# Performance work log

Measured on AMD Instinct MI355X. Metric: run time of the kernel, lower is better.

## Reference

```python
import jax, jax.numpy as jnp
import numpy as np

B, T, C = 32, 128, 64
E, H = 8, 4            # feat_dim, num_heads
D = E // H             # head_dim = 2
HID = 32               # hidden_dim


def setup_inputs() -> dict:
    key = jax.random.key(0)
    ks = jax.random.split(key, 20)
    s = 0.1
    return {
        "x": jax.random.normal(ks[0], (B, T, C), jnp.float32),
        # input_proj: Linear(C, C)
        "W_in": jax.random.normal(ks[1], (C, C), jnp.float32) * s,
        "b_in": jax.random.normal(ks[2], (C,), jnp.float32) * s,
        # time_step_score: Linear(C, C//4) -> GELU -> Linear(C//4, 1) -> Sigmoid
        "W_ts1": jax.random.normal(ks[3], (C // 4, C), jnp.float32) * s,
        "b_ts1": jax.random.normal(ks[4], (C // 4,), jnp.float32) * s,
        "W_ts2": jax.random.normal(ks[5], (1, C // 4), jnp.float32) * s,
        "b_ts2": jax.random.normal(ks[6], (1,), jnp.float32) * s,
        # per-channel GRU(1 -> E): torch gate order (r, z, n)
        "W_ih": jax.random.normal(ks[7], (C, 3 * E), jnp.float32) * s,      # input size 1
        "W_hh": jax.random.normal(ks[8], (C, 3 * E, E), jnp.float32) * s,
        "b_ih": jax.random.normal(ks[9], (C, 3 * E), jnp.float32) * s,
        "b_hh": jax.random.normal(ks[10], (C, 3 * E), jnp.float32) * s,
        # shared MultiheadAttention(E, 4): packed in_proj + out_proj
        "W_qkv": jax.random.normal(ks[11], (3 * E, E), jnp.float32) * s,
        "b_qkv": jax.random.normal(ks[12], (3 * E,), jnp.float32) * s,
        "W_o": jax.random.normal(ks[13], (E, E), jnp.float32) * s,
        "b_o": jax.random.normal(ks[14], (E,), jnp.float32) * s,
        # out_proj: Linear(C*E, HID)
        "W_out": jax.random.normal(ks[15], (HID, C * E), jnp.float32) * s,
        "b_out": jax.random.normal(ks[16], (HID,), jnp.float32) * s,
    }


def _forward(x, W_in, b_in, W_ts1, b_ts1, W_ts2, b_ts2,
             W_ih, W_hh, b_ih, b_hh, W_qkv, b_qkv, W_o, b_o, W_out, b_out):
    bs, ts, c = x.shape
    # time step importance: per-timestep MLP over the raw features
    h1 = jax.nn.gelu(jnp.einsum('btc,fc->btf', x, W_ts1) + b_ts1, approximate=False)
    ts_imp = jax.nn.sigmoid(jnp.einsum('btf,of->bto', h1, W_ts2) + b_ts2)[..., 0]  # [B,T]

    xp = jnp.einsum('btc,dc->btd', x, W_in) + b_in  # [B,T,C]

    # Batched per-channel GRU scan over time. state h: [B,C,E]
    def step(h, x_t):
        gi = x_t[:, :, None] * W_ih[None] + b_ih          # [B,C,3E]
        gh = jnp.einsum('bce,cge->bcg', h, W_hh) + b_hh   # [B,C,3E]
        ir, iz, inn = gi[..., :E], gi[..., E:2 * E], gi[..., 2 * E:]
        hr, hz, hn = gh[..., :E], gh[..., E:2 * E], gh[..., 2 * E:]
        r = jax.nn.sigmoid(ir + hr)
        z = jax.nn.sigmoid(iz + hz)
        n = jnp.tanh(inn + r * hn)
        h_new = (1.0 - z) * n + z * h
        return h_new, h_new

    h0 = jnp.zeros((bs, c, E), xp.dtype)
    _, hs = jax.lax.scan(step, h0, jnp.transpose(xp, (1, 0, 2)))  # [T,B,C,E]
    hs_bcte = jnp.transpose(hs, (1, 2, 0, 3))                     # [B,C,T,E]

    # Shared MHA applied independently per channel (batched over B*C)
    qkv = jnp.einsum('bcte,fe->bctf', hs_bcte, W_qkv) + b_qkv     # [B,C,T,3E]
    q, k, v = qkv[..., :E], qkv[..., E:2 * E], qkv[..., 2 * E:]
    def heads(t):
        return t.reshape(bs, c, ts, H, D)
    q, k, v = heads(q), heads(k), heads(v)
    scores = jnp.einsum('bcthd,bcshd->bchts', q, k) / np.sqrt(D)
    attn = jax.nn.softmax(scores, axis=-1)
    o = jnp.einsum('bchts,bcshd->bcthd', attn, v).reshape(bs, c, ts, E)
    attn_out = jnp.einsum('bcte,fe->bctf', o, W_o) + b_o          # [B,C,T,E]
    attention = jnp.transpose(attn_out, (0, 2, 1, 3))             # [B,T,C,E]

    out_flat = jnp.transpose(hs, (1, 0, 2, 3)).reshape(bs, ts, c * E)  # [B,T,C*E]
    out = jnp.einsum('btf,hf->bth', out_flat, W_out) + b_out           # [B,T,HID]

    feat_imp = jax.nn.sigmoid(attention.sum(axis=(1, 3)))   # [B,C]
    tsf_imp = jax.nn.sigmoid(attention.sum(axis=-1))        # [B,T,C]
    return out[:, -1, :], feat_imp, ts_imp, tsf_imp


def reference(x, W_in, b_in, W_ts1, b_ts1, W_ts2, b_ts2,
              W_ih, W_hh, b_ih, b_hh, W_qkv, b_qkv, W_o, b_o, W_out, b_out):
    return _forward(x, W_in, b_in, W_ts1, b_ts1, W_ts2, b_ts2,
                    W_ih, W_hh, b_ih, b_hh, W_qkv, b_qkv, W_o, b_o, W_out, b_out)
```

## Files before the change

### kernel.cpp

```cpp
#include <hip/hip_runtime.h>
#include <hip/hip_bf16.h>
#include <math.h>

#define B_ 32
#define T_ 128
#define C_ 64
#define E_ 8
#define HID_ 32

__device__ __forceinline__ float sigmoidf_(float x) { return 1.0f / (1.0f + __expf(-x)); }
__device__ __forceinline__ float tanhf_(float x) {
    float xc = fminf(fmaxf(x, -15.0f), 15.0f);
    float e = __expf(2.0f * xc);
    return (e - 1.0f) / (e + 1.0f);
}

__global__ __launch_bounds__(128) void k_attn_f(
    const float* __restrict__ x, const float* __restrict__ W_in, const float* __restrict__ b_in,
    const float* __restrict__ W_ih, const float* __restrict__ W_hh,
    const float* __restrict__ b_ih, const float* __restrict__ b_hh,
    const float* __restrict__ W_qkv, const float* __restrict__ b_qkv,
    const float* __restrict__ W_o, const float* __restrict__ b_o,
    float* __restrict__ fh,
    float* __restrict__ feat_imp, float* __restrict__ tsf_imp)
{
    const int bc = blockIdx.x;
    const int b = bc >> 6, c = bc & 63;
    const int tid = threadIdx.x;

    __shared__ __align__(16) float ks[T_][E_];
    __shared__ __align__(16) float vs[T_][E_];
    __shared__ __align__(16) float hsl[T_][E_];
    __shared__ __align__(16) float xcol[T_];
    __shared__ __align__(16) float win_c[C_];

    if (tid < C_) win_c[tid] = W_in[c * C_ + tid];
    __syncthreads();

    {
        float a = b_in[c];
        const float4* xr = (const float4*)(x + (b * T_ + tid) * C_);
        const float4* wv4 = (const float4*)win_c;
#pragma unroll
        for (int k4 = 0; k4 < 16; ++k4) {
            float4 xv = xr[k4];
            float4 wv = wv4[k4];
            a = fmaf(xv.x, wv.x, a); a = fmaf(xv.y, wv.y, a);
            a = fmaf(xv.z, wv.z, a); a = fmaf(xv.w, wv.w, a);
        }
        xcol[tid] = a;
    }
    __syncthreads();

    if (tid < E_) {
        const int e = tid;
        float wr[E_], wz[E_], wn[E_];
#pragma unroll
        for (int j = 0; j < E_; ++j) {
            wr[j] = W_hh[(c * 24 + 0 * E_ + e) * E_ + j];
            wz[j] = W_hh[(c * 24 + 1 * E_ + e) * E_ + j];
            wn[j] = W_hh[(c * 24 + 2 * E_ + e) * E_ + j];
        }
        const float wir = W_ih[c * 24 + e], wiz = W_ih[c * 24 + E_ + e], win = W_ih[c * 24 + 2 * E_ + e];
        const float bir = b_ih[c * 24 + e], biz = b_ih[c * 24 + E_ + e], bin_ = b_ih[c * 24 + 2 * E_ + e];
        const float bhr = b_hh[c * 24 + e], bhz = b_hh[c * 24 + E_ + e], bhn = b_hh[c * 24 + 2 * E_ + e];

        float h = 0.0f;
        for (int t = 0; t < T_; ++t) {
            float xv = xcol[t];
            float gr = fmaf(xv, wir, bir) + bhr;
            float gz = fmaf(xv, wiz, biz) + bhz;
            float gn = fmaf(xv, win, bin_);
            float hn = bhn;
#pragma unroll
            for (int j = 0; j < E_; ++j) {
                float hj = __shfl(h, j, E_);
                gr = fmaf(hj, wr[j], gr);
                gz = fmaf(hj, wz[j], gz);
                hn = fmaf(hj, wn[j], hn);
            }
            float r = sigmoidf_(gr);
            float z = sigmoidf_(gz);
            float nn = tanhf_(fmaf(r, hn, gn));
            h = (1.0f - z) * nn + z * h;
            hsl[t][e] = h;
        }
        fh[bc * E_ + e] = h;
    }
    __syncthreads();

    const int t = tid;
    float hrow[E_];
#pragma unroll
    for (int j = 0; j < E_; ++j) hrow[j] = hsl[t][j];

    float q[E_];
#pragma unroll
    for (int f = 0; f < E_; ++f) {
        float a = b_qkv[f];
#pragma unroll
        for (int j = 0; j < E_; ++j) a = fmaf(hrow[j], W_qkv[f * E_ + j], a);
        q[f] = a;
    }
#pragma unroll
    for (int f = 0; f < E_; ++f) {
        float a = b_qkv[E_ + f];
#pragma unroll
        for (int j = 0; j < E_; ++j) a = fmaf(hrow[j], W_qkv[(E_ + f) * E_ + j], a);
        ks[t][f] = a;
    }
#pragma unroll
    for (int f = 0; f < E_; ++f) {
        float a = b_qkv[2 * E_ + f];
#pragma unroll
        for (int j = 0; j < E_; ++j) a = fmaf(hrow[j], W_qkv[(2 * E_ + f) * E_ + j], a);
        vs[t][f] = a;
    }
    __syncthreads();

    const float scale = 0.70710678118654752f;
    float l[4] = {0.f, 0.f, 0.f, 0.f};
    float acc[E_] = {0.f, 0.f, 0.f, 0.f, 0.f, 0.f, 0.f, 0.f};
    for (int s = 0; s < T_; ++s) {
        float4 k0 = *(const float4*)&ks[s][0];
        float4 k1 = *(const float4*)&ks[s][4];
        float4 v0 = *(const float4*)&vs[s][0];
        float4 v1 = *(const float4*)&vs[s][4];
        float p0 = __expf((q[0] * k0.x + q[1] * k0.y) * scale);
        float p1 = __expf((q[2] * k0.z + q[3] * k0.w) * scale);
        float p2 = __expf((q[4] * k1.x + q[5] * k1.y) * scale);
        float p3 = __expf((q[6] * k1.z + q[7] * k1.w) * scale);
        l[0] += p0; l[1] += p1; l[2] += p2; l[3] += p3;
        acc[0] = fmaf(p0, v0.x, acc[0]); acc[1] = fmaf(p0, v0.y, acc[1]);
        acc[2] = fmaf(p1, v0.z, acc[2]); acc[3] = fmaf(p1, v0.w, acc[3]);
        acc[4] = fmaf(p2, v1.x, acc[4]); acc[5] = fmaf(p2, v1.y, acc[5]);
        acc[6] = fmaf(p3, v1.z, acc[6]); acc[7] = fmaf(p3, v1.w, acc[7]);
    }

    float S = 0.0f;
#pragma unroll
    for (int f = 0; f < E_; ++f) {
        float wsum = 0.0f;
#pragma unroll
        for (int fp = 0; fp < E_; ++fp) wsum += W_o[fp * E_ + f];
        S = fmaf(acc[f] / l[f >> 1], wsum, S);
    }
#pragma unroll
    for (int fp = 0; fp < E_; ++fp) S += b_o[fp];

    tsf_imp[(size_t)b * T_ * C_ + (size_t)t * C_ + c] = sigmoidf_(S);

    float* red = xcol;
    red[t] = S;
    __syncthreads();
    for (int off = 64; off > 0; off >>= 1) {
        if (t < off) red[t] += red[t + off];
        __syncthreads();
    }
    if (t == 0) feat_imp[bc] = sigmoidf_(red[0]);
}

__global__ __launch_bounds__(64) void k_ts(
    const float* __restrict__ x,
    const float* __restrict__ W_ts1, const float* __restrict__ b_ts1,
    const float* __restrict__ W_ts2, const float* __restrict__ b_ts2,
    float* __restrict__ ts_imp)
{
    const int bt = blockIdx.x;
    const int tid = threadIdx.x;
    __shared__ float xs[C_];
    __shared__ float h1[16];
    xs[tid] = x[bt * C_ + tid];
    __syncthreads();
    if (tid < 16) {
        float a = b_ts1[tid];
#pragma unroll
        for (int k = 0; k < C_; ++k) a = fmaf(xs[k], W_ts1[tid * C_ + k], a);
        h1[tid] = 0.5f * a * (1.0f + erff(a * 0.70710678118654752f));
    }
    __syncthreads();
    if (tid == 0) {
        float s = b_ts2[0];
#pragma unroll
        for (int k = 0; k < 16; ++k) s = fmaf(h1[k], W_ts2[k], s);
        ts_imp[bt] = sigmoidf_(s);
    }
}

__global__ __launch_bounds__(64) void k_out(
    const float* __restrict__ fh, const float* __restrict__ W_out, const float* __restrict__ b_out,
    float* __restrict__ out0)
{
    const int b = blockIdx.x;
    const int tid = threadIdx.x;
    __shared__ float hf[C_ * E_];
    const float4* src = (const float4*)(fh + (b * C_ + tid) * E_);
    float4* dst = (float4*)(hf + tid * E_);
    dst[0] = src[0];
    dst[1] = src[1];
    __syncthreads();
    if (tid < HID_) {
        float a = b_out[tid];
        const float* wo = W_out + tid * (C_ * E_);
        for (int k = 0; k < C_ * E_; ++k) a = fmaf(hf[k], wo[k], a);
        out0[b * HID_ + tid] = a;
    }
}

extern "C" void kernel_launch(void* const* d_in, const int* in_sizes, int n_in,
                              void* d_out, int out_size, void* d_ws, size_t ws_size,
                              hipStream_t stream) {
    (void)in_sizes; (void)n_in; (void)out_size; (void)ws_size;

    float* out0 = (float*)d_out;
    float* feat = out0 + B_ * HID_;
    float* tsim = feat + B_ * C_;
    float* tsf  = tsim + B_ * T_;

    const float* x     = (const float*)d_in[0];
    const float* W_in  = (const float*)d_in[1];
    const float* b_in  = (const float*)d_in[2];
    const float* W_ts1 = (const float*)d_in[3];
    const float* b_ts1 = (const float*)d_in[4];
    const float* W_ts2 = (const float*)d_in[5];
    const float* b_ts2 = (const float*)d_in[6];
    const float* W_ih  = (const float*)d_in[7];
    const float* W_hh  = (const float*)d_in[8];
    const float* b_ih  = (const float*)d_in[9];
    const float* b_hh  = (const float*)d_in[10];
    const float* W_qkv = (const float*)d_in[11];
    const float* b_qkv = (const float*)d_in[12];
    const float* W_o   = (const float*)d_in[13];
    const float* b_o   = (const float*)d_in[14];
    const float* W_out = (const float*)d_in[15];
    const float* b_out = (const float*)d_in[16];

    float* fhb = (float*)d_ws;

    hipLaunchKernelGGL(k_attn_f, dim3(B_ * C_), dim3(128), 0, stream,
                       x, W_in, b_in, W_ih, W_hh, b_ih, b_hh,
                       W_qkv, b_qkv, W_o, b_o, fhb, feat, tsf);
    hipLaunchKernelGGL(k_ts, dim3(B_ * T_), dim3(64), 0, stream,
                       x, W_ts1, b_ts1, W_ts2, b_ts2, tsim);
    hipLaunchKernelGGL(k_out, dim3(B_), dim3(64), 0, stream,
                       fhb, W_out, b_out, out0);
}
```

Measured before the change: 95.67 us.

## Split fused attention kernel into input-projection, packed GRU, and attention kernels

Breaks the monolithic per-(b,c) kernel into three stages. k_pre computes the input projection. k_gru packs 8 GRU chains into one 64-thread wavefront, so all lanes run recurrences instead of 8 of 128 threads while the rest sit idle. k_attn then reads the hidden states from global memory. The softmax scale is also folded with log2(e) into q so the inner loop can use exp2f. This trades two extra launches and global round-trips of xp and hs for far better lane utilisation on the serial GRU scan.

```diff
diff --git a/kernel.cpp b/kernel.cpp
--- a/kernel.cpp
+++ b/kernel.cpp
@@ -15,92 +15,111 @@
     return (e - 1.0f) / (e + 1.0f);
 }
 
-__global__ __launch_bounds__(128) void k_attn_f(
+__global__ __launch_bounds__(64) void k_pre(
     const float* __restrict__ x, const float* __restrict__ W_in, const float* __restrict__ b_in,
-    const float* __restrict__ W_ih, const float* __restrict__ W_hh,
+    float* __restrict__ xp)
+{
+    const int bt = blockIdx.x;
+    const int tid = threadIdx.x;
+    __shared__ __align__(16) float4 xs4[16];
+    if (tid < 16) xs4[tid] = ((const float4*)(x + bt * C_))[tid];
+    __syncthreads();
+    float a = b_in[tid];
+    const float4* w4 = (const float4*)(W_in + tid * C_);
+#pragma unroll
+    for (int k4 = 0; k4 < 16; ++k4) {
+        float4 xv = xs4[k4];
+        float4 wv = w4[k4];
+        a = fmaf(xv.x, wv.x, a); a = fmaf(xv.y, wv.y, a);
+        a = fmaf(xv.z, wv.z, a); a = fmaf(xv.w, wv.w, a);
+    }
+    xp[bt * C_ + tid] = a;
+}
+
+__global__ __launch_bounds__(64) void k_gru(
+    const float* __restrict__ xp, const float* __restrict__ W_ih, const float* __restrict__ W_hh,
     const float* __restrict__ b_ih, const float* __restrict__ b_hh,
-    const float* __restrict__ W_qkv, const float* __restrict__ b_qkv,
+    float* __restrict__ hs, float* __restrict__ fh)
+{
+    const int tid = threadIdx.x;
+    const int ci = tid >> 3;
+    const int e = tid & 7;
+    const int chain = blockIdx.x * 8 + ci;
+    const int b = chain >> 6;
+    const int c = chain & 63;
+
+    __shared__ float xc[8][T_ + 1];
+
+    for (int tt = 0; tt < 16; ++tt) {
+        const int t = e * 16 + tt;
+        xc[ci][t] = xp[(b * T_ + t) * C_ + c];
+    }
+    __syncthreads();
+
+    float wr[E_], wz[E_], wn[E_];
+#pragma unroll
+    for (int j = 0; j < E_; ++j) {
+        wr[j] = W_hh[(c * 24 + 0 * E_ + e) * E_ + j];
+        wz[j] = W_hh[(c * 24 + 1 * E_ + e) * E_ + j];
+        wn[j] = W_hh[(c * 24 + 2 * E_ + e) * E_ + j];
+    }
+    const float wir = W_ih[c * 24 + e], wiz = W_ih[c * 24 + E_ + e], win = W_ih[c * 24 + 2 * E_ + e];
+    const float bir = b_ih[c * 24 + e], biz = b_ih[c * 24 + E_ + e], bin_ = b_ih[c * 24 + 2 * E_ + e];
+    const float bhr = b_hh[c * 24 + e], bhz = b_hh[c * 24 + E_ + e], bhn = b_hh[c * 24 + 2 * E_ + e];
+
+    float h = 0.0f;
+    float* ho = hs + (size_t)chain * T_ * E_ + e;
+    for (int t = 0; t < T_; ++t) {
+        float xv = xc[ci][t];
+        float gr = fmaf(xv, wir, bir) + bhr;
+        float gz = fmaf(xv, wiz, biz) + bhz;
+        float gn = fmaf(xv, win, bin_);
+        float hn = bhn;
+#pragma unroll
+        for (int j = 0; j < E_; ++j) {
+            float hj = __shfl(h, j, E_);
+            gr = fmaf(hj, wr[j], gr);
+            gz = fmaf(hj, wz[j], gz);
+            hn = fmaf(hj, wn[j], hn);
+        }
+        float r = sigmoidf_(gr);
+        float z = sigmoidf_(gz);
+        float nn = tanhf_(fmaf(r, hn, gn));
+        h = (1.0f - z) * nn + z * h;
+        ho[t * E_] = h;
+    }
+    fh[chain * E_ + e] = h;
+}
+
+__global__ __launch_bounds__(128) void k_attn(
+    const float* __restrict__ hs, const float* __restrict__ W_qkv, const float* __restrict__ b_qkv,
     const float* __restrict__ W_o, const float* __restrict__ b_o,
-    float* __restrict__ fh,
     float* __restrict__ feat_imp, float* __restrict__ tsf_imp)
 {
     const int bc = blockIdx.x;
     const int b = bc >> 6, c = bc & 63;
-    const int tid = threadIdx.x;
+    const int t = threadIdx.x;
 
     __shared__ __align__(16) float ks[T_][E_];
     __shared__ __align__(16) float vs[T_][E_];
-    __shared__ __align__(16) float hsl[T_][E_];
-    __shared__ __align__(16) float xcol[T_];
-    __shared__ __align__(16) float win_c[C_];
-
-    if (tid < C_) win_c[tid] = W_in[c * C_ + tid];
-    __syncthreads();
-
+    __shared__ float red[T_];
+
+    float hrow[E_];
     {
-        float a = b_in[c];
-        const float4* xr = (const float4*)(x + (b * T_ + tid) * C_);
-        const float4* wv4 = (const float4*)win_c;
-#pragma unroll
-        for (int k4 = 0; k4 < 16; ++k4) {
-            float4 xv = xr[k4];
-            float4 wv = wv4[k4];
-            a = fmaf(xv.x, wv.x, a); a = fmaf(xv.y, wv.y, a);
-            a = fmaf(xv.z, wv.z, a); a = fmaf(xv.w, wv.w, a);
-        }
-        xcol[tid] = a;
-    }
-    __syncthreads();
-
-    if (tid < E_) {
-        const int e = tid;
-        float wr[E_], wz[E_], wn[E_];
-#pragma unroll
-        for (int j = 0; j < E_; ++j) {
-            wr[j] = W_hh[(c * 24 + 0 * E_ + e) * E_ + j];
-            wz[j] = W_hh[(c * 24 + 1 * E_ + e) * E_ + j];
-            wn[j] = W_hh[(c * 24 + 2 * E_ + e) * E_ + j];
-        }
-        const float wir = W_ih[c * 24 + e], wiz = W_ih[c * 24 + E_ + e], win = W_ih[c * 24 + 2 * E_ + e];
-        const float bir = b_ih[c * 24 + e], biz = b_ih[c * 24 + E_ + e], bin_ = b_ih[c * 24 + 2 * E_ + e];
-        const float bhr = b_hh[c * 24 + e], bhz = b_hh[c * 24 + E_ + e], bhn = b_hh[c * 24 + 2 * E_ + e];
-
-        float h = 0.0f;
-        for (int t = 0; t < T_; ++t) {
-            float xv = xcol[t];
-            float gr = fmaf(xv, wir, bir) + bhr;
-            float gz = fmaf(xv, wiz, biz) + bhz;
-            float gn = fmaf(xv, win, bin_);
-            float hn = bhn;
-#pragma unroll
-            for (int j = 0; j < E_; ++j) {
-                float hj = __shfl(h, j, E_);
-                gr = fmaf(hj, wr[j], gr);
-                gz = fmaf(hj, wz[j], gz);
-                hn = fmaf(hj, wn[j], hn);
-            }
-            float r = sigmoidf_(gr);
-            float z = sigmoidf_(gz);
-            float nn = tanhf_(fmaf(r, hn, gn));
-            h = (1.0f - z) * nn + z * h;
-            hsl[t][e] = h;
-        }
-        fh[bc * E_ + e] = h;
-    }
-    __syncthreads();
-
-    const int t = tid;
-    float hrow[E_];
-#pragma unroll
-    for (int j = 0; j < E_; ++j) hrow[j] = hsl[t][j];
-
+        const float4* hp = (const float4*)(hs + (size_t)bc * T_ * E_ + t * E_);
+        float4 h0 = hp[0], h1 = hp[1];
+        hrow[0] = h0.x; hrow[1] = h0.y; hrow[2] = h0.z; hrow[3] = h0.w;
+        hrow[4] = h1.x; hrow[5] = h1.y; hrow[6] = h1.z; hrow[7] = h1.w;
+    }
+
+    const float qscale = 0.70710678118654752f * 1.44269504088896341f;
     float q[E_];
 #pragma unroll
     for (int f = 0; f < E_; ++f) {
         float a = b_qkv[f];
 #pragma unroll
         for (int j = 0; j < E_; ++j) a = fmaf(hrow[j], W_qkv[f * E_ + j], a);
-        q[f] = a;
+        q[f] = a * qscale;
     }
 #pragma unroll
     for (int f = 0; f < E_; ++f) {
@@ -118,7 +137,6 @@
     }
     __syncthreads();
 
-    const float scale = 0.70710678118654752f;
     float l[4] = {0.f, 0.f, 0.f, 0.f};
     float acc[E_] = {0.f, 0.f, 0.f, 0.f, 0.f, 0.f, 0.f, 0.f};
     for (int s = 0; s < T_; ++s) {
@@ -126,10 +144,10 @@
         float4 k1 = *(const float4*)&ks[s][4];
         float4 v0 = *(const float4*)&vs[s][0];
         float4 v1 = *(const float4*)&vs[s][4];
-        float p0 = __expf((q[0] * k0.x + q[1] * k0.y) * scale);
-        float p1 = __expf((q[2] * k0.z + q[3] * k0.w) * scale);
-        float p2 = __expf((q[4] * k1.x + q[5] * k1.y) * scale);
-        float p3 = __expf((q[6] * k1.z + q[7] * k1.w) * scale);
+        float p0 = exp2f(fmaf(q[1], k0.y, q[0] * k0.x));
+        float p1 = exp2f(fmaf(q[3], k0.w, q[2] * k0.z));
+        float p2 = exp2f(fmaf(q[5], k1.y, q[4] * k1.x));
+        float p3 = exp2f(fmaf(q[7], k1.w, q[6] * k1.z));
         l[0] += p0; l[1] += p1; l[2] += p2; l[3] += p3;
         acc[0] = fmaf(p0, v0.x, acc[0]); acc[1] = fmaf(p0, v0.y, acc[1]);
         acc[2] = fmaf(p1, v0.z, acc[2]); acc[3] = fmaf(p1, v0.w, acc[3]);
@@ -150,7 +168,6 @@
 
     tsf_imp[(size_t)b * T_ * C_ + (size_t)t * C_ + c] = sigmoidf_(S);
 
-    float* red = xcol;
     red[t] = S;
     __syncthreads();
     for (int off = 64; off > 0; off >>= 1) {
@@ -236,10 +253,14 @@
     const float* b_out = (const float*)d_in[16];
 
     float* fhb = (float*)d_ws;
-
-    hipLaunchKernelGGL(k_attn_f, dim3(B_ * C_), dim3(128), 0, stream,
-                       x, W_in, b_in, W_ih, W_hh, b_ih, b_hh,
-                       W_qkv, b_qkv, W_o, b_o, fhb, feat, tsf);
+    float* xpb = fhb + B_ * C_ * E_;
+    float* hsb = xpb + (size_t)B_ * T_ * C_;
+
+    hipLaunchKernelGGL(k_pre, dim3(B_ * T_), dim3(64), 0, stream, x, W_in, b_in, xpb);
+    hipLaunchKernelGGL(k_gru, dim3(B_ * C_ / 8), dim3(64), 0, stream,
+                       xpb, W_ih, W_hh, b_ih, b_hh, hsb, fhb);
+    hipLaunchKernelGGL(k_attn, dim3(B_ * C_), dim3(128), 0, stream,
+                       hsb, W_qkv, b_qkv, W_o, b_o, feat, tsf);
     hipLaunchKernelGGL(k_ts, dim3(B_ * T_), dim3(64), 0, stream,
                        x, W_ts1, b_ts1, W_ts2, b_ts2, tsim);
     hipLaunchKernelGGL(k_out, dim3(B_), dim3(64), 0, stream,
```

After: 103.9 us. +8.6%, slower.
